# Optimization experiments

Hardware: AMD Instinct MI355X
Metric: run time of the kernel (lower is better)

Reference implementation:

```python
import jax, jax.numpy as jnp
import numpy as np

N = 100000       # nodes
D = 256          # input_dim
H = 256          # hidden = min(2*D, 256)
O = 256          # output_dim
MAXDEG = 16
BN_EPS = 1e-5


def setup_inputs() -> dict:
    key = jax.random.key(0)
    ks = jax.random.split(key, 6)
    x = jax.random.normal(ks[0], (N, D), dtype=jnp.float32)
    padded_neighbors = jax.random.randint(ks[1], (N, MAXDEG), 0, N, dtype=jnp.int32)
    W1 = jax.random.normal(ks[2], (D, H), dtype=jnp.float32) * (1.0 / np.sqrt(D))
    b1 = jnp.zeros((H,), jnp.float32)
    W2 = jax.random.normal(ks[3], (H, O), dtype=jnp.float32) * (1.0 / np.sqrt(H))
    b2 = jnp.zeros((O,), jnp.float32)
    gamma = jnp.ones((O,), jnp.float32)
    beta = jnp.zeros((O,), jnp.float32)
    alpha = jnp.float32(0.1)   # Parameter init in 'mean_max' branch
    eps = jnp.float32(0.0)     # learnable eps, init 0.0
    return {"x": x, "padded_neighbors": padded_neighbors, "W1": W1, "b1": b1,
            "W2": W2, "b2": b2, "gamma": gamma, "beta": beta,
            "alpha": alpha, "eps": eps}


def max_pooling_gin(h, padded_neighbors):
    # dummy row = columnwise min; index -1 maps to the dummy row (torch's h[-1])
    dummy = jnp.min(h, axis=0, keepdims=True)          # (1, D)
    h_with_dummy = jnp.concatenate([h, dummy], axis=0)  # (N+1, D)
    idx = jnp.where(padded_neighbors < 0, h.shape[0], padded_neighbors)
    return jnp.max(h_with_dummy[idx], axis=1)           # (N, D)


def reference(x, padded_neighbors, W1, b1, W2, b2, gamma, beta, alpha, eps):
    # --- aggregation: mean over neighbors (== spmm with binary adj / degree) ---
    mask = padded_neighbors >= 0                         # (N, deg)
    idx = jnp.where(mask, padded_neighbors, 0)
    gathered = x[idx] * mask[..., None].astype(x.dtype)  # (N, deg, D)
    neigh_sum = gathered.sum(axis=1)                     # (N, D)
    degree = mask.sum(axis=1, keepdims=True).astype(x.dtype)
    h = neigh_sum / degree
    # --- '_max' branch: add alpha * gather-max of aggregated features ---
    h = h + alpha * max_pooling_gin(h, padded_neighbors)
    # --- self connection + eps residual ---
    h = h + x + eps * x
    # --- backbone: Linear-ReLU-Linear-ReLU-BatchNorm1d (training-mode stats) ---
    h = jax.nn.relu(h @ W1 + b1)
    h = jax.nn.relu(h @ W2 + b2)
    mean = h.mean(axis=0)
    var = h.var(axis=0)  # biased variance, as torch BN uses for normalization
    out = (h - mean) * jax.lax.rsqrt(var + BN_EPS) * gamma + beta
    return out
```

## Files before the change

### kernel.cpp

```cpp
#include <hip/hip_runtime.h>

typedef __bf16 bf16x8 __attribute__((ext_vector_type(8)));
typedef float  f32x4  __attribute__((ext_vector_type(4)));
typedef _Float16 h2v  __attribute__((ext_vector_type(2)));

__device__ __forceinline__ unsigned short f2bf(float f) {
  unsigned u = __builtin_bit_cast(unsigned, f);
  u += 0x7FFFu + ((u >> 16) & 1u);
  return (unsigned short)(u >> 16);
}
__device__ __forceinline__ float bf2f(unsigned short b) {
  unsigned u = ((unsigned)b) << 16;
  return __builtin_bit_cast(float, u);
}
__device__ __forceinline__ float bflo(unsigned q) {
  return __builtin_bit_cast(float, q << 16);
}
__device__ __forceinline__ float bfhi(unsigned q) {
  return __builtin_bit_cast(float, q & 0xFFFF0000u);
}
__device__ __forceinline__ unsigned pack2bf(float lo, float hi) {
  return (unsigned)f2bf(lo) | ((unsigned)f2bf(hi) << 16);
}

__device__ __forceinline__ float fp8raw(unsigned byte) {
  unsigned b = ((byte & 0x80u) << 24) | ((byte & 0x7Fu) << 20);
  return __builtin_bit_cast(float, b);
}
__device__ __forceinline__ unsigned f2fp8(float v) {
  unsigned b = __builtin_bit_cast(unsigned, v);
  unsigned sg = (b >> 24) & 0x80u;
  float a = __builtin_bit_cast(float, b & 0x7FFFFFFFu) * 0x1p-120f;
  unsigned ab = __builtin_bit_cast(unsigned, a);
  ab += 0x7FFFFu + ((ab >> 20) & 1u);
  return sg | ((ab >> 20) & 0x7Fu);
}
__device__ __forceinline__ h2v pkL(unsigned w) {
  unsigned x = ((w << 8) & 0x80008000u) | ((w << 7) & 0x3F803F80u);
  return __builtin_bit_cast(h2v, x);
}
__device__ __forceinline__ h2v pkH(unsigned w) {
  unsigned x = (w & 0x80008000u) | ((w >> 1) & 0x3F803F80u);
  return __builtin_bit_cast(h2v, x);
}
__device__ __forceinline__ h2v shfl32(h2v a) {
  return __builtin_bit_cast(h2v,
      __shfl_xor(__builtin_bit_cast(unsigned, a), 32));
}

__global__ __launch_bounds__(256) void x2bf_kernel(
    const float* __restrict__ x, unsigned short* __restrict__ xh,
    unsigned char* __restrict__ xq, int total8)
{
  const int i = blockIdx.x * 256 + threadIdx.x;
  if (i >= total8) return;
  const float4* p = (const float4*)x + (long)i * 2;
  float4 a = p[0], b = p[1];
  uint4 o;
  o.x = pack2bf(a.x, a.y); o.y = pack2bf(a.z, a.w);
  o.z = pack2bf(b.x, b.y); o.w = pack2bf(b.z, b.w);
  ((uint4*)xh)[i] = o;
  uint2 q;
  q.x = f2fp8(a.x) | (f2fp8(a.y) << 8) | (f2fp8(a.z) << 16) | (f2fp8(a.w) << 24);
  q.y = f2fp8(b.x) | (f2fp8(b.y) << 8) | (f2fp8(b.z) << 16) | (f2fp8(b.w) << 24);
  ((uint2*)xq)[i] = q;
}

__global__ __launch_bounds__(256) void prep_kernel(
    const float* __restrict__ W1, const float* __restrict__ W2,
    unsigned short* __restrict__ Wt1, unsigned short* __restrict__ Wt2)
{
  const int n = blockIdx.x;
  const int k = threadIdx.x;
  Wt1[n * 256 + k] = f2bf(W1[k * 256 + n]);
  Wt2[n * 256 + k] = f2bf(W2[k * 256 + n]);
}

__global__ __launch_bounds__(256) void aggregate_kernel(
    const unsigned char* __restrict__ xq, const int* __restrict__ nbr,
    unsigned short* __restrict__ h0, unsigned char* __restrict__ h0q, int N)
{
  const int wid  = (blockIdx.x * 256 + threadIdx.x) >> 6;
  const int lane = threadIdx.x & 63;
  if (wid >= N) return;
  const int half = lane >> 5;
  const int l    = lane & 31;
  const int* nb = nbr + (long)wid * 16;
  int4 n0 = ((const int4*)nb)[half * 2];
  int4 n1 = ((const int4*)nb)[half * 2 + 1];
  int v[8] = {n0.x, n0.y, n0.z, n0.w, n1.x, n1.y, n1.z, n1.w};
  int mn = v[0];
#pragma unroll
  for (int t = 1; t < 8; ++t) mn = min(mn, v[t]);

  if (__all(mn >= 0)) {
    uint2 vals[8];
#pragma unroll
    for (int t = 0; t < 8; ++t)
      vals[t] = ((const uint2*)(xq + (long)v[t] * 256))[l];
    h2v s02 = (h2v)0, s13 = (h2v)0, s46 = (h2v)0, s57 = (h2v)0;
#pragma unroll
    for (int t = 0; t < 8; ++t) {
      s02 = s02 + pkL(vals[t].x);
      s13 = s13 + pkH(vals[t].x);
      s46 = s46 + pkL(vals[t].y);
      s57 = s57 + pkH(vals[t].y);
    }
    s02 = s02 + shfl32(s02);
    s13 = s13 + shfl32(s13);
    s46 = s46 + shfl32(s46);
    s57 = s57 + shfl32(s57);
    if (half == 0) {
      float m[8];
      m[0] = (float)s02[0] * 16.f; m[2] = (float)s02[1] * 16.f;
      m[1] = (float)s13[0] * 16.f; m[3] = (float)s13[1] * 16.f;
      m[4] = (float)s46[0] * 16.f; m[6] = (float)s46[1] * 16.f;
      m[5] = (float)s57[0] * 16.f; m[7] = (float)s57[1] * 16.f;
      uint4 o;
      o.x = pack2bf(m[0], m[1]); o.y = pack2bf(m[2], m[3]);
      o.z = pack2bf(m[4], m[5]); o.w = pack2bf(m[6], m[7]);
      ((uint4*)(h0 + (long)wid * 256))[l] = o;
      uint2 q;
      q.x = f2fp8(m[0]) | (f2fp8(m[1]) << 8) | (f2fp8(m[2]) << 16) | (f2fp8(m[3]) << 24);
      q.y = f2fp8(m[4]) | (f2fp8(m[5]) << 8) | (f2fp8(m[6]) << 16) | (f2fp8(m[7]) << 24);
      ((uint2*)(h0q + (long)wid * 256))[l] = q;
    }
    return;
  }
  float wgt[8]; int idx[8];
#pragma unroll
  for (int t = 0; t < 8; ++t) {
    wgt[t] = (v[t] >= 0) ? 1.0f : 0.0f;
    idx[t] = (v[t] >= 0) ? v[t] : 0;
  }
  uint2 vals[8];
#pragma unroll
  for (int t = 0; t < 8; ++t)
    vals[t] = ((const uint2*)(xq + (long)idx[t] * 256))[l];
  float s[8] = {0.f,0.f,0.f,0.f,0.f,0.f,0.f,0.f};
  float cnt = 0.f;
#pragma unroll
  for (int t = 0; t < 8; ++t) {
    const unsigned w0 = vals[t].x, w1 = vals[t].y;
    cnt += wgt[t];
    s[0] = fmaf(wgt[t], fp8raw(w0 & 0xFF), s[0]);
    s[1] = fmaf(wgt[t], fp8raw((w0 >> 8) & 0xFF), s[1]);
    s[2] = fmaf(wgt[t], fp8raw((w0 >> 16) & 0xFF), s[2]);
    s[3] = fmaf(wgt[t], fp8raw(w0 >> 24), s[3]);
    s[4] = fmaf(wgt[t], fp8raw(w1 & 0xFF), s[4]);
    s[5] = fmaf(wgt[t], fp8raw((w1 >> 8) & 0xFF), s[5]);
    s[6] = fmaf(wgt[t], fp8raw((w1 >> 16) & 0xFF), s[6]);
    s[7] = fmaf(wgt[t], fp8raw(w1 >> 24), s[7]);
  }
#pragma unroll
  for (int e = 0; e < 8; ++e) s[e] += __shfl_xor(s[e], 32);
  cnt += __shfl_xor(cnt, 32);
  const float inv = cnt > 0.f ? 0x1p120f / cnt : 0.f;
  if (half == 0) {
    float m[8];
#pragma unroll
    for (int e = 0; e < 8; ++e) m[e] = s[e] * inv;
    uint4 o;
    o.x = pack2bf(m[0], m[1]); o.y = pack2bf(m[2], m[3]);
    o.z = pack2bf(m[4], m[5]); o.w = pack2bf(m[6], m[7]);
    ((uint4*)(h0 + (long)wid * 256))[l] = o;
    uint2 q;
    q.x = f2fp8(m[0]) | (f2fp8(m[1]) << 8) | (f2fp8(m[2]) << 16) | (f2fp8(m[3]) << 24);
    q.y = f2fp8(m[4]) | (f2fp8(m[5]) << 8) | (f2fp8(m[6]) << 16) | (f2fp8(m[7]) << 24);
    ((uint2*)(h0q + (long)wid * 256))[l] = q;
  }
}

__global__ __launch_bounds__(256) void combine_kernel(
    const unsigned short* __restrict__ h0, const unsigned char* __restrict__ h0q,
    const int* __restrict__ nbr, const unsigned short* __restrict__ xh,
    const float* __restrict__ alpha_p, const float* __restrict__ eps_p,
    unsigned short* __restrict__ h1, int N)
{
  const int wid  = (blockIdx.x * 256 + threadIdx.x) >> 6;
  const int lane = threadIdx.x & 63;
  if (wid >= N) return;
  const int half = lane >> 5;
  const int l    = lane & 31;
  const float alpha = *alpha_p;
  const float c     = 1.0f + *eps_p;
  const int* nb = nbr + (long)wid * 16;
  int4 n0 = ((const int4*)nb)[half * 2];
  int4 n1 = ((const int4*)nb)[half * 2 + 1];
  int v[8] = {n0.x, n0.y, n0.z, n0.w, n1.x, n1.y, n1.z, n1.w};
  int mn = v[0];
#pragma unroll
  for (int t = 1; t < 8; ++t) mn = min(mn, v[t]);

  uint4 own = ((const uint4*)(h0 + (long)wid * 256))[l];
  uint4 xv  = ((const uint4*)(xh + (long)wid * 256))[l];

  if (__all(mn >= 0)) {
    uint2 vals[8];
#pragma unroll
    for (int t = 0; t < 8; ++t)
      vals[t] = ((const uint2*)(h0q + (long)v[t] * 256))[l];
    const h2v NEG2 = __builtin_bit_cast(h2v, 0xFC00FC00u);
    h2v m02 = NEG2, m13 = NEG2, m46 = NEG2, m57 = NEG2;
#pragma unroll
    for (int t = 0; t < 8; ++t) {
      m02 = __builtin_elementwise_max(m02, pkL(vals[t].x));
      m13 = __builtin_elementwise_max(m13, pkH(vals[t].x));
      m46 = __builtin_elementwise_max(m46, pkL(vals[t].y));
      m57 = __builtin_elementwise_max(m57, pkH(vals[t].y));
    }
    m02 = __builtin_elementwise_max(m02, shfl32(m02));
    m13 = __builtin_elementwise_max(m13, shfl32(m13));
    m46 = __builtin_elementwise_max(m46, shfl32(m46));
    m57 = __builtin_elementwise_max(m57, shfl32(m57));
    if (half == 0) {
      float mx[8];
      mx[0] = (float)m02[0] * 256.f; mx[2] = (float)m02[1] * 256.f;
      mx[1] = (float)m13[0] * 256.f; mx[3] = (float)m13[1] * 256.f;
      mx[4] = (float)m46[0] * 256.f; mx[6] = (float)m46[1] * 256.f;
      mx[5] = (float)m57[0] * 256.f; mx[7] = (float)m57[1] * 256.f;
      const unsigned* qo = (const unsigned*)&own;
      const unsigned* qx = (const unsigned*)&xv;
      uint4 o;
      unsigned* q = (unsigned*)&o;
#pragma unroll
      for (int w = 0; w < 4; ++w) {
        float rl = bflo(qo[w]) + alpha * mx[2*w]   + c * bflo(qx[w]);
        float rh = bfhi(qo[w]) + alpha * mx[2*w+1] + c * bfhi(qx[w]);
        q[w] = pack2bf(rl, rh);
      }
      ((uint4*)(h1 + (long)wid * 256))[l] = o;
    }
    return;
  }
  float mx[8];
#pragma unroll
  for (int e = 0; e < 8; ++e) mx[e] = -3.402823466e38f;
  {
    float wgt[8]; int idx[8];
#pragma unroll
    for (int t = 0; t < 8; ++t) {
      wgt[t] = (v[t] >= 0) ? 1.0f : 0.0f;
      idx[t] = (v[t] >= 0) ? v[t] : 0;
    }
    uint2 vals[8];
#pragma unroll
    for (int t = 0; t < 8; ++t)
      vals[t] = ((const uint2*)(h0q + (long)idx[t] * 256))[l];
#pragma unroll
    for (int t = 0; t < 8; ++t) {
      const unsigned w0 = vals[t].x, w1 = vals[t].y;
      const bool valid = wgt[t] > 0.f;
      const float NEG = -3.402823466e38f;
      mx[0] = fmaxf(mx[0], valid ? fp8raw(w0 & 0xFF) * 0x1p120f : NEG);
      mx[1] = fmaxf(mx[1], valid ? fp8raw((w0 >> 8) & 0xFF) * 0x1p120f : NEG);
      mx[2] = fmaxf(mx[2], valid ? fp8raw((w0 >> 16) & 0xFF) * 0x1p120f : NEG);
      mx[3] = fmaxf(mx[3], valid ? fp8raw(w0 >> 24) * 0x1p120f : NEG);
      mx[4] = fmaxf(mx[4], valid ? fp8raw(w1 & 0xFF) * 0x1p120f : NEG);
      mx[5] = fmaxf(mx[5], valid ? fp8raw((w1 >> 8) & 0xFF) * 0x1p120f : NEG);
      mx[6] = fmaxf(mx[6], valid ? fp8raw((w1 >> 16) & 0xFF) * 0x1p120f : NEG);
      mx[7] = fmaxf(mx[7], valid ? fp8raw(w1 >> 24) * 0x1p120f : NEG);
    }
  }
#pragma unroll
  for (int e = 0; e < 8; ++e) mx[e] = fmaxf(mx[e], __shfl_xor(mx[e], 32));
  if (half == 0) {
    const unsigned* qo = (const unsigned*)&own;
    const unsigned* qx = (const unsigned*)&xv;
    uint4 o;
    unsigned* q = (unsigned*)&o;
#pragma unroll
    for (int w = 0; w < 4; ++w) {
      float rl = bflo(qo[w]) + alpha * mx[2*w]   + c * bflo(qx[w]);
      float rh = bfhi(qo[w]) + alpha * mx[2*w+1] + c * bfhi(qx[w]);
      q[w] = pack2bf(rl, rh);
    }
    ((uint4*)(h1 + (long)wid * 256))[l] = o;
  }
}

template<int WITH_STATS>
__global__ __launch_bounds__(512, 2) void gemm_w_kernel(
    const unsigned short* __restrict__ A, const unsigned short* __restrict__ Wt,
    const float* __restrict__ bias, unsigned short* __restrict__ Out,
    float* __restrict__ partials, int M, int ntiles)
{
  __shared__ __align__(16) unsigned short lW[256 * 256];
  const int tid  = threadIdx.x;
  const int lane = tid & 63;
  const int wave = tid >> 6;
  const int wrh  = wave >> 2;
  const int wc   = wave & 3;
  const int g = lane >> 4, lr = lane & 15;
  char* lWc = (char*)lW;

  {
    const int row   = tid >> 1;
    const int cbase = (tid & 1) * 256;
    const char* src = (const char*)Wt + row * 512 + cbase;
#pragma unroll
    for (int i = 0; i < 16; ++i) {
      uint4 v = *(const uint4*)(src + i * 16);
      *(uint4*)(lWc + ((row * 512 + cbase + i * 16) ^ ((row & 7) << 4))) = v;
    }
  }
  __syncthreads();

  float bv[4];
#pragma unroll
  for (int nt = 0; nt < 4; ++nt) bv[nt] = bias[wc * 64 + nt * 16 + lr];

  float s[4] = {0.f, 0.f, 0.f, 0.f}, s2[4] = {0.f, 0.f, 0.f, 0.f};
  const char* Ab = (const char*)A;

  for (int tile = blockIdx.x; tile < ntiles; tile += gridDim.x) {
    const long row0 = (long)tile * 128;
    f32x4 acc[4][4] = {};
    const long abase = (row0 + wrh * 64 + lr) * 512 + g * 16;
#pragma unroll
    for (int kk = 0; kk < 8; ++kk) {
      bf16x8 af[4], bq[4];
#pragma unroll
      for (int mt = 0; mt < 4; ++mt)
        af[mt] = *(const bf16x8*)(Ab + abase + mt * (16 * 512) + kk * 64);
#pragma unroll
      for (int nt = 0; nt < 4; ++nt) {
        const int wrow = wc * 64 + nt * 16 + lr;
        bq[nt] = *(const bf16x8*)(lWc +
                   ((wrow * 512 + kk * 64 + g * 16) ^ ((wrow & 7) << 4)));
      }
#pragma unroll
      for (int mt = 0; mt < 4; ++mt)
#pragma unroll
        for (int nt = 0; nt < 4; ++nt)
          acc[mt][nt] = __builtin_amdgcn_mfma_f32_16x16x32_bf16(
              af[mt], bq[nt], acc[mt][nt], 0, 0, 0);
    }
#pragma unroll
    for (int nt = 0; nt < 4; ++nt) {
      const int col = wc * 64 + nt * 16 + lr;
#pragma unroll
      for (int mt = 0; mt < 4; ++mt) {
        f32x4 vv = acc[mt][nt];
        const long rbase = row0 + wrh * 64 + mt * 16 + g * 4;
#pragma unroll
        for (int e = 0; e < 4; ++e) {
          const float val = fmaxf(vv[e] + bv[nt], 0.f);
          Out[(rbase + e) * 256 + col] = f2bf(val);
          if (WITH_STATS) {
            if (rbase + e < M) { s[nt] += val; s2[nt] += val * val; }
          }
        }
      }
    }
  }

  if (WITH_STATS) {
#pragma unroll
    for (int nt = 0; nt < 4; ++nt) {
      s[nt]  += __shfl_xor(s[nt], 16);   s2[nt] += __shfl_xor(s2[nt], 16);
      s[nt]  += __shfl_xor(s[nt], 32);   s2[nt] += __shfl_xor(s2[nt], 32);
    }
    if (g == 0) {
      float* p = partials + (blockIdx.x * 2 + wrh) * 512;
#pragma unroll
      for (int nt = 0; nt < 4; ++nt) {
        const int col = wc * 64 + nt * 16 + lr;
        p[col]       = s[nt];
        p[256 + col] = s2[nt];
      }
    }
  }
}

__global__ __launch_bounds__(256) void bn_finalize_kernel(
    const float* __restrict__ gamma, const float* __restrict__ beta,
    const float* __restrict__ partials, float* __restrict__ stats, int M)
{
  const int n = threadIdx.x;
  float s = 0.f, s2 = 0.f;
  for (int b = 0; b < 512; ++b) {
    s  += partials[b * 512 + n];
    s2 += partials[b * 512 + 256 + n];
  }
  const float invM = 1.0f / (float)M;
  const float mean = s * invM;
  float var = s2 * invM - mean * mean;
  var = fmaxf(var, 0.f);
  const float sc = gamma[n] * rsqrtf(var + 1e-5f);
  stats[512 + n] = sc;
  stats[768 + n] = beta[n] - mean * sc;
}

__global__ __launch_bounds__(256) void bn_norm_kernel(
    const unsigned short* __restrict__ h3, const float* __restrict__ stats,
    float* __restrict__ out, int total8)
{
  const int i = blockIdx.x * 256 + threadIdx.x;
  if (i >= total8) return;
  uint4 v = ((const uint4*)h3)[i];
  const int c = (i * 8) & 255;
  const float4 sc0 = *(const float4*)&stats[512 + c];
  const float4 sc1 = *(const float4*)&stats[516 + c];
  const float4 sh0 = *(const float4*)&stats[768 + c];
  const float4 sh1 = *(const float4*)&stats[772 + c];
  const unsigned short* u = (const unsigned short*)&v;
  float4 o0, o1;
  o0.x = bf2f(u[0]) * sc0.x + sh0.x;
  o0.y = bf2f(u[1]) * sc0.y + sh0.y;
  o0.z = bf2f(u[2]) * sc0.z + sh0.z;
  o0.w = bf2f(u[3]) * sc0.w + sh0.w;
  o1.x = bf2f(u[4]) * sc1.x + sh1.x;
  o1.y = bf2f(u[5]) * sc1.y + sh1.y;
  o1.z = bf2f(u[6]) * sc1.z + sh1.z;
  o1.w = bf2f(u[7]) * sc1.w + sh1.w;
  ((float4*)out)[2 * i]     = o0;
  ((float4*)out)[2 * i + 1] = o1;
}

extern "C" void kernel_launch(void* const* d_in, const int* in_sizes, int n_in,
                              void* d_out, int out_size, void* d_ws, size_t ws_size,
                              hipStream_t stream) {
  const float* x     = (const float*)d_in[0];
  const int*   nbr   = (const int*)d_in[1];
  const float* W1    = (const float*)d_in[2];
  const float* b1    = (const float*)d_in[3];
  const float* W2    = (const float*)d_in[4];
  const float* b2    = (const float*)d_in[5];
  const float* gamma = (const float*)d_in[6];
  const float* beta  = (const float*)d_in[7];
  const float* alpha_p = (const float*)d_in[8];
  const float* eps_p   = (const float*)d_in[9];
  float* out = (float*)d_out;

  const int  N  = in_sizes[0] / 256;
  const long MP = ((long)N + 127) & ~127L;
  const int  ntiles = (int)(MP / 128);

  unsigned short* xh   = (unsigned short*)d_ws;
  unsigned short* bufA = xh + MP * 256;
  unsigned short* bufB = bufA + MP * 256;
  unsigned short* Wt1  = bufB + MP * 256;
  unsigned short* Wt2  = Wt1 + 256 * 256;
  unsigned char*  h0q  = (unsigned char*)(Wt2 + 256 * 256);
  float* partials = (float*)(h0q + MP * 256);
  float* stats    = partials + 512 * 512;
  unsigned char*  xq = (unsigned char*)bufB;

  x2bf_kernel<<<(N * 32 + 255) / 256, 256, 0, stream>>>(x, xh, xq, N * 32);
  prep_kernel<<<256, 256, 0, stream>>>(W1, W2, Wt1, Wt2);
  aggregate_kernel<<<(N + 3) / 4, 256, 0, stream>>>(xq, nbr, bufA, h0q, N);
  combine_kernel<<<(N + 3) / 4, 256, 0, stream>>>(bufA, h0q, nbr, xh,
                                                  alpha_p, eps_p, bufB, N);

  gemm_w_kernel<0><<<256, 512, 0, stream>>>(bufB, Wt1, b1, xh, nullptr, N, ntiles);
  gemm_w_kernel<1><<<256, 512, 0, stream>>>(xh, Wt2, b2, bufA, partials, N, ntiles);

  bn_finalize_kernel<<<1, 256, 0, stream>>>(gamma, beta, partials, stats, N);
  bn_norm_kernel<<<(N * 32 + 255) / 256, 256, 0, stream>>>(bufA, stats, out, N * 32);
}
```

Measured before the change: 319.8 us.

## Drop bf16 aggregate buffer and widen GEMM blocks to 16 waves

The aggregate kernel no longer writes a bf16 copy of the mean-aggregated features. The combine kernel reconstructs its own row from the fp8 buffer, which cuts one write and one read of a full N×256 bf16 tensor. Separately, the GEMM kernels now launch 1024 threads per block (16 waves), each computing a 64×32 output slice instead of 64×64. That halves per-wave accumulator registers and spreads the weight-tile load over more threads. The costs are lower precision in the self term (fp8 instead of bf16) and a launch_bounds of (1024,4) that may constrain registers or occupancy.

```diff
diff --git a/kernel.cpp b/kernel.cpp
--- a/kernel.cpp
+++ b/kernel.cpp
@@ -78,7 +78,7 @@
 
 __global__ __launch_bounds__(256) void aggregate_kernel(
     const unsigned char* __restrict__ xq, const int* __restrict__ nbr,
-    unsigned short* __restrict__ h0, unsigned char* __restrict__ h0q, int N)
+    unsigned char* __restrict__ h0q, int N)
 {
   const int wid  = (blockIdx.x * 256 + threadIdx.x) >> 6;
   const int lane = threadIdx.x & 63;
@@ -116,10 +116,6 @@
       m[1] = (float)s13[0] * 16.f; m[3] = (float)s13[1] * 16.f;
       m[4] = (float)s46[0] * 16.f; m[6] = (float)s46[1] * 16.f;
       m[5] = (float)s57[0] * 16.f; m[7] = (float)s57[1] * 16.f;
-      uint4 o;
-      o.x = pack2bf(m[0], m[1]); o.y = pack2bf(m[2], m[3]);
-      o.z = pack2bf(m[4], m[5]); o.w = pack2bf(m[6], m[7]);
-      ((uint4*)(h0 + (long)wid * 256))[l] = o;
       uint2 q;
       q.x = f2fp8(m[0]) | (f2fp8(m[1]) << 8) | (f2fp8(m[2]) << 16) | (f2fp8(m[3]) << 24);
       q.y = f2fp8(m[4]) | (f2fp8(m[5]) << 8) | (f2fp8(m[6]) << 16) | (f2fp8(m[7]) << 24);
@@ -160,10 +156,6 @@
     float m[8];
 #pragma unroll
     for (int e = 0; e < 8; ++e) m[e] = s[e] * inv;
-    uint4 o;
-    o.x = pack2bf(m[0], m[1]); o.y = pack2bf(m[2], m[3]);
-    o.z = pack2bf(m[4], m[5]); o.w = pack2bf(m[6], m[7]);
-    ((uint4*)(h0 + (long)wid * 256))[l] = o;
     uint2 q;
     q.x = f2fp8(m[0]) | (f2fp8(m[1]) << 8) | (f2fp8(m[2]) << 16) | (f2fp8(m[3]) << 24);
     q.y = f2fp8(m[4]) | (f2fp8(m[5]) << 8) | (f2fp8(m[6]) << 16) | (f2fp8(m[7]) << 24);
@@ -172,10 +164,9 @@
 }
 
 __global__ __launch_bounds__(256) void combine_kernel(
-    const unsigned short* __restrict__ h0, const unsigned char* __restrict__ h0q,
-    const int* __restrict__ nbr, const unsigned short* __restrict__ xh,
-    const float* __restrict__ alpha_p, const float* __restrict__ eps_p,
-    unsigned short* __restrict__ h1, int N)
+    const unsigned char* __restrict__ h0q, const int* __restrict__ nbr,
+    const unsigned short* __restrict__ xh, const float* __restrict__ alpha_p,
+    const float* __restrict__ eps_p, unsigned short* __restrict__ h1, int N)
 {
   const int wid  = (blockIdx.x * 256 + threadIdx.x) >> 6;
   const int lane = threadIdx.x & 63;
@@ -192,8 +183,8 @@
 #pragma unroll
   for (int t = 1; t < 8; ++t) mn = min(mn, v[t]);
 
-  uint4 own = ((const uint4*)(h0 + (long)wid * 256))[l];
-  uint4 xv  = ((const uint4*)(xh + (long)wid * 256))[l];
+  uint2 ownq = ((const uint2*)(h0q + (long)wid * 256))[l];
+  uint4 xv   = ((const uint4*)(xh + (long)wid * 256))[l];
 
   if (__all(mn >= 0)) {
     uint2 vals[8];
@@ -219,14 +210,20 @@
       mx[1] = (float)m13[0] * 256.f; mx[3] = (float)m13[1] * 256.f;
       mx[4] = (float)m46[0] * 256.f; mx[6] = (float)m46[1] * 256.f;
       mx[5] = (float)m57[0] * 256.f; mx[7] = (float)m57[1] * 256.f;
-      const unsigned* qo = (const unsigned*)&own;
+      h2v o02 = pkL(ownq.x), o13 = pkH(ownq.x);
+      h2v o46 = pkL(ownq.y), o57 = pkH(ownq.y);
+      float ov[8];
+      ov[0] = (float)o02[0] * 256.f; ov[2] = (float)o02[1] * 256.f;
+      ov[1] = (float)o13[0] * 256.f; ov[3] = (float)o13[1] * 256.f;
+      ov[4] = (float)o46[0] * 256.f; ov[6] = (float)o46[1] * 256.f;
+      ov[5] = (float)o57[0] * 256.f; ov[7] = (float)o57[1] * 256.f;
       const unsigned* qx = (const unsigned*)&xv;
       uint4 o;
       unsigned* q = (unsigned*)&o;
 #pragma unroll
       for (int w = 0; w < 4; ++w) {
-        float rl = bflo(qo[w]) + alpha * mx[2*w]   + c * bflo(qx[w]);
-        float rh = bfhi(qo[w]) + alpha * mx[2*w+1] + c * bfhi(qx[w]);
+        float rl = ov[2*w]   + alpha * mx[2*w]   + c * bflo(qx[w]);
+        float rh = ov[2*w+1] + alpha * mx[2*w+1] + c * bfhi(qx[w]);
         q[w] = pack2bf(rl, rh);
       }
       ((uint4*)(h1 + (long)wid * 256))[l] = o;
@@ -265,14 +262,22 @@
 #pragma unroll
   for (int e = 0; e < 8; ++e) mx[e] = fmaxf(mx[e], __shfl_xor(mx[e], 32));
   if (half == 0) {
-    const unsigned* qo = (const unsigned*)&own;
+    float ov[8];
+    ov[0] = fp8raw(ownq.x & 0xFF) * 0x1p120f;
+    ov[1] = fp8raw((ownq.x >> 8) & 0xFF) * 0x1p120f;
+    ov[2] = fp8raw((ownq.x >> 16) & 0xFF) * 0x1p120f;
+    ov[3] = fp8raw(ownq.x >> 24) * 0x1p120f;
+    ov[4] = fp8raw(ownq.y & 0xFF) * 0x1p120f;
+    ov[5] = fp8raw((ownq.y >> 8) & 0xFF) * 0x1p120f;
+    ov[6] = fp8raw((ownq.y >> 16) & 0xFF) * 0x1p120f;
+    ov[7] = fp8raw(ownq.y >> 24) * 0x1p120f;
     const unsigned* qx = (const unsigned*)&xv;
     uint4 o;
     unsigned* q = (unsigned*)&o;
 #pragma unroll
     for (int w = 0; w < 4; ++w) {
-      float rl = bflo(qo[w]) + alpha * mx[2*w]   + c * bflo(qx[w]);
-      float rh = bfhi(qo[w]) + alpha * mx[2*w+1] + c * bfhi(qx[w]);
+      float rl = ov[2*w]   + alpha * mx[2*w]   + c * bflo(qx[w]);
+      float rh = ov[2*w+1] + alpha * mx[2*w+1] + c * bfhi(qx[w]);
       q[w] = pack2bf(rl, rh);
     }
     ((uint4*)(h1 + (long)wid * 256))[l] = o;
@@ -280,7 +285,7 @@
 }
 
 template<int WITH_STATS>
-__global__ __launch_bounds__(512, 2) void gemm_w_kernel(
+__global__ __launch_bounds__(1024, 4) void gemm_w_kernel(
     const unsigned short* __restrict__ A, const unsigned short* __restrict__ Wt,
     const float* __restrict__ bias, unsigned short* __restrict__ Out,
     float* __restrict__ partials, int M, int ntiles)
@@ -289,56 +294,56 @@
   const int tid  = threadIdx.x;
   const int lane = tid & 63;
   const int wave = tid >> 6;
-  const int wrh  = wave >> 2;
-  const int wc   = wave & 3;
+  const int wrh  = wave >> 3;
+  const int wc   = wave & 7;
   const int g = lane >> 4, lr = lane & 15;
   char* lWc = (char*)lW;
 
   {
-    const int row   = tid >> 1;
-    const int cbase = (tid & 1) * 256;
+    const int row   = tid >> 2;
+    const int cbase = (tid & 3) * 128;
     const char* src = (const char*)Wt + row * 512 + cbase;
 #pragma unroll
-    for (int i = 0; i < 16; ++i) {
+    for (int i = 0; i < 8; ++i) {
       uint4 v = *(const uint4*)(src + i * 16);
       *(uint4*)(lWc + ((row * 512 + cbase + i * 16) ^ ((row & 7) << 4))) = v;
     }
   }
   __syncthreads();
 
-  float bv[4];
-#pragma unroll
-  for (int nt = 0; nt < 4; ++nt) bv[nt] = bias[wc * 64 + nt * 16 + lr];
-
-  float s[4] = {0.f, 0.f, 0.f, 0.f}, s2[4] = {0.f, 0.f, 0.f, 0.f};
+  float bv[2];
+#pragma unroll
+  for (int nt = 0; nt < 2; ++nt) bv[nt] = bias[wc * 32 + nt * 16 + lr];
+
+  float s[2] = {0.f, 0.f}, s2[2] = {0.f, 0.f};
   const char* Ab = (const char*)A;
 
   for (int tile = blockIdx.x; tile < ntiles; tile += gridDim.x) {
     const long row0 = (long)tile * 128;
-    f32x4 acc[4][4] = {};
+    f32x4 acc[4][2] = {};
     const long abase = (row0 + wrh * 64 + lr) * 512 + g * 16;
 #pragma unroll
     for (int kk = 0; kk < 8; ++kk) {
-      bf16x8 af[4], bq[4];
+      bf16x8 af[4], bq[2];
 #pragma unroll
       for (int mt = 0; mt < 4; ++mt)
         af[mt] = *(const bf16x8*)(Ab + abase + mt * (16 * 512) + kk * 64);
 #pragma unroll
-      for (int nt = 0; nt < 4; ++nt) {
-        const int wrow = wc * 64 + nt * 16 + lr;
+      for (int nt = 0; nt < 2; ++nt) {
+        const int wrow = wc * 32 + nt * 16 + lr;
         bq[nt] = *(const bf16x8*)(lWc +
                    ((wrow * 512 + kk * 64 + g * 16) ^ ((wrow & 7) << 4)));
       }
 #pragma unroll
       for (int mt = 0; mt < 4; ++mt)
 #pragma unroll
-        for (int nt = 0; nt < 4; ++nt)
+        for (int nt = 0; nt < 2; ++nt)
           acc[mt][nt] = __builtin_amdgcn_mfma_f32_16x16x32_bf16(
               af[mt], bq[nt], acc[mt][nt], 0, 0, 0);
     }
 #pragma unroll
-    for (int nt = 0; nt < 4; ++nt) {
-      const int col = wc * 64 + nt * 16 + lr;
+    for (int nt = 0; nt < 2; ++nt) {
+      const int col = wc * 32 + nt * 16 + lr;
 #pragma unroll
       for (int mt = 0; mt < 4; ++mt) {
         f32x4 vv = acc[mt][nt];
@@ -357,15 +362,15 @@
 
   if (WITH_STATS) {
 #pragma unroll
-    for (int nt = 0; nt < 4; ++nt) {
+    for (int nt = 0; nt < 2; ++nt) {
       s[nt]  += __shfl_xor(s[nt], 16);   s2[nt] += __shfl_xor(s2[nt], 16);
       s[nt]  += __shfl_xor(s[nt], 32);   s2[nt] += __shfl_xor(s2[nt], 32);
     }
     if (g == 0) {
       float* p = partials + (blockIdx.x * 2 + wrh) * 512;
 #pragma unroll
-      for (int nt = 0; nt < 4; ++nt) {
-        const int col = wc * 64 + nt * 16 + lr;
+      for (int nt = 0; nt < 2; ++nt) {
+        const int col = wc * 32 + nt * 16 + lr;
         p[col]       = s[nt];
         p[256 + col] = s2[nt];
       }
@@ -449,12 +454,12 @@
 
   x2bf_kernel<<<(N * 32 + 255) / 256, 256, 0, stream>>>(x, xh, xq, N * 32);
   prep_kernel<<<256, 256, 0, stream>>>(W1, W2, Wt1, Wt2);
-  aggregate_kernel<<<(N + 3) / 4, 256, 0, stream>>>(xq, nbr, bufA, h0q, N);
-  combine_kernel<<<(N + 3) / 4, 256, 0, stream>>>(bufA, h0q, nbr, xh,
+  aggregate_kernel<<<(N + 3) / 4, 256, 0, stream>>>(xq, nbr, h0q, N);
+  combine_kernel<<<(N + 3) / 4, 256, 0, stream>>>(h0q, nbr, xh,
                                                   alpha_p, eps_p, bufB, N);
 
-  gemm_w_kernel<0><<<256, 512, 0, stream>>>(bufB, Wt1, b1, xh, nullptr, N, ntiles);
-  gemm_w_kernel<1><<<256, 512, 0, stream>>>(xh, Wt2, b2, bufA, partials, N, ntiles);
+  gemm_w_kernel<0><<<256, 1024, 0, stream>>>(bufB, Wt1, b1, xh, nullptr, N, ntiles);
+  gemm_w_kernel<1><<<256, 1024, 0, stream>>>(xh, Wt2, b2, bufA, partials, N, ntiles);
 
   bn_finalize_kernel<<<1, 256, 0, stream>>>(gamma, beta, partials, stats, N);
   bn_norm_kernel<<<(N * 32 + 255) / 256, 256, 0, stream>>>(bufA, stats, out, N * 32);
```

New measurement: 365.3 us. 1.14x slower.

## Retile GEMMs to 256-row by 128-column tiles with one tile per block

Applied to the files above, without the earlier changes.

Drops the persistent 256-block grid and gives each block one 256-row by half-width (128-column) tile, launching 2*ntiles blocks. Each block now stages only half of W in LDS, so the 128 KB buffer becomes 64 KB and launch bounds rise to allow four blocks per CU. The BN partial-sum layout and the finalize reduction change to match. The aim is better occupancy and load balance across the MI355X CUs. In exchange, each block reloads half of W from global memory, and the A rows are read twice, once per column half, which adds traffic.

```diff
diff --git a/kernel.cpp b/kernel.cpp
--- a/kernel.cpp
+++ b/kernel.cpp
@@ -280,26 +280,28 @@
 }
 
 template<int WITH_STATS>
-__global__ __launch_bounds__(512, 2) void gemm_w_kernel(
+__global__ __launch_bounds__(512, 4) void gemm_w_kernel(
     const unsigned short* __restrict__ A, const unsigned short* __restrict__ Wt,
     const float* __restrict__ bias, unsigned short* __restrict__ Out,
-    float* __restrict__ partials, int M, int ntiles)
-{
-  __shared__ __align__(16) unsigned short lW[256 * 256];
+    float* __restrict__ partials, int M)
+{
+  __shared__ __align__(16) unsigned short lW[128 * 256];
   const int tid  = threadIdx.x;
   const int lane = tid & 63;
   const int wave = tid >> 6;
-  const int wrh  = wave >> 2;
-  const int wc   = wave & 3;
+  const int wm   = wave >> 1;
+  const int wn   = wave & 1;
   const int g = lane >> 4, lr = lane & 15;
+  const int colhalf = blockIdx.x & 1;
+  const long row0   = (long)(blockIdx.x >> 1) * 256;
   char* lWc = (char*)lW;
 
   {
-    const int row   = tid >> 1;
-    const int cbase = (tid & 1) * 256;
-    const char* src = (const char*)Wt + row * 512 + cbase;
-#pragma unroll
-    for (int i = 0; i < 16; ++i) {
+    const int row   = tid >> 2;
+    const int cbase = (tid & 3) * 128;
+    const char* src = (const char*)Wt + (long)(colhalf * 128 + row) * 512 + cbase;
+#pragma unroll
+    for (int i = 0; i < 8; ++i) {
       uint4 v = *(const uint4*)(src + i * 16);
       *(uint4*)(lWc + ((row * 512 + cbase + i * 16) ^ ((row & 7) << 4))) = v;
     }
@@ -308,48 +310,47 @@
 
   float bv[4];
 #pragma unroll
-  for (int nt = 0; nt < 4; ++nt) bv[nt] = bias[wc * 64 + nt * 16 + lr];
+  for (int nt = 0; nt < 4; ++nt)
+    bv[nt] = bias[colhalf * 128 + wn * 64 + nt * 16 + lr];
 
   float s[4] = {0.f, 0.f, 0.f, 0.f}, s2[4] = {0.f, 0.f, 0.f, 0.f};
   const char* Ab = (const char*)A;
 
-  for (int tile = blockIdx.x; tile < ntiles; tile += gridDim.x) {
-    const long row0 = (long)tile * 128;
-    f32x4 acc[4][4] = {};
-    const long abase = (row0 + wrh * 64 + lr) * 512 + g * 16;
-#pragma unroll
-    for (int kk = 0; kk < 8; ++kk) {
-      bf16x8 af[4], bq[4];
-#pragma unroll
-      for (int mt = 0; mt < 4; ++mt)
-        af[mt] = *(const bf16x8*)(Ab + abase + mt * (16 * 512) + kk * 64);
-#pragma unroll
-      for (int nt = 0; nt < 4; ++nt) {
-        const int wrow = wc * 64 + nt * 16 + lr;
-        bq[nt] = *(const bf16x8*)(lWc +
-                   ((wrow * 512 + kk * 64 + g * 16) ^ ((wrow & 7) << 4)));
-      }
-#pragma unroll
-      for (int mt = 0; mt < 4; ++mt)
-#pragma unroll
-        for (int nt = 0; nt < 4; ++nt)
-          acc[mt][nt] = __builtin_amdgcn_mfma_f32_16x16x32_bf16(
-              af[mt], bq[nt], acc[mt][nt], 0, 0, 0);
-    }
+  f32x4 acc[4][4] = {};
+  const long abase = (row0 + wm * 64 + lr) * 512 + g * 16;
+#pragma unroll
+  for (int kk = 0; kk < 8; ++kk) {
+    bf16x8 af[4], bq[4];
+#pragma unroll
+    for (int mt = 0; mt < 4; ++mt)
+      af[mt] = *(const bf16x8*)(Ab + abase + mt * (16 * 512) + kk * 64);
 #pragma unroll
     for (int nt = 0; nt < 4; ++nt) {
-      const int col = wc * 64 + nt * 16 + lr;
-#pragma unroll
-      for (int mt = 0; mt < 4; ++mt) {
-        f32x4 vv = acc[mt][nt];
-        const long rbase = row0 + wrh * 64 + mt * 16 + g * 4;
-#pragma unroll
-        for (int e = 0; e < 4; ++e) {
-          const float val = fmaxf(vv[e] + bv[nt], 0.f);
-          Out[(rbase + e) * 256 + col] = f2bf(val);
-          if (WITH_STATS) {
-            if (rbase + e < M) { s[nt] += val; s2[nt] += val * val; }
-          }
+      const int wrow = wn * 64 + nt * 16 + lr;
+      bq[nt] = *(const bf16x8*)(lWc +
+                 ((wrow * 512 + kk * 64 + g * 16) ^ ((wrow & 7) << 4)));
+    }
+#pragma unroll
+    for (int mt = 0; mt < 4; ++mt)
+#pragma unroll
+      for (int nt = 0; nt < 4; ++nt)
+        acc[mt][nt] = __builtin_amdgcn_mfma_f32_16x16x32_bf16(
+            af[mt], bq[nt], acc[mt][nt], 0, 0, 0);
+  }
+
+#pragma unroll
+  for (int nt = 0; nt < 4; ++nt) {
+    const int col = colhalf * 128 + wn * 64 + nt * 16 + lr;
+#pragma unroll
+    for (int mt = 0; mt < 4; ++mt) {
+      f32x4 vv = acc[mt][nt];
+      const long rbase = row0 + wm * 64 + mt * 16 + g * 4;
+#pragma unroll
+      for (int e = 0; e < 4; ++e) {
+        const float val = fmaxf(vv[e] + bv[nt], 0.f);
+        Out[(rbase + e) * 256 + col] = f2bf(val);
+        if (WITH_STATS) {
+          if (rbase + e < M) { s[nt] += val; s2[nt] += val * val; }
         }
       }
     }
@@ -362,12 +363,12 @@
       s[nt]  += __shfl_xor(s[nt], 32);   s2[nt] += __shfl_xor(s2[nt], 32);
     }
     if (g == 0) {
-      float* p = partials + (blockIdx.x * 2 + wrh) * 512;
+      float* p = partials + ((long)blockIdx.x * 4 + wm) * 256;
 #pragma unroll
       for (int nt = 0; nt < 4; ++nt) {
-        const int col = wc * 64 + nt * 16 + lr;
-        p[col]       = s[nt];
-        p[256 + col] = s2[nt];
+        const int cl = wn * 64 + nt * 16 + lr;
+        p[cl]       = s[nt];
+        p[128 + cl] = s2[nt];
       }
     }
   }
@@ -375,13 +376,21 @@
 
 __global__ __launch_bounds__(256) void bn_finalize_kernel(
     const float* __restrict__ gamma, const float* __restrict__ beta,
-    const float* __restrict__ partials, float* __restrict__ stats, int M)
-{
-  const int n = threadIdx.x;
+    const float* __restrict__ partials, float* __restrict__ stats,
+    int M, int ntiles)
+{
+  const int n  = threadIdx.x;
+  const int ch = n >> 7;
+  const int cl = n & 127;
   float s = 0.f, s2 = 0.f;
-  for (int b = 0; b < 512; ++b) {
-    s  += partials[b * 512 + n];
-    s2 += partials[b * 512 + 256 + n];
+  for (int k = 0; k < ntiles; ++k) {
+    const long bid = (long)(2 * k + ch);
+    const float* p = partials + bid * 4 * 256;
+#pragma unroll
+    for (int wm = 0; wm < 4; ++wm) {
+      s  += p[wm * 256 + cl];
+      s2 += p[wm * 256 + 128 + cl];
+    }
   }
   const float invM = 1.0f / (float)M;
   const float mean = s * invM;
@@ -434,8 +443,8 @@
   float* out = (float*)d_out;
 
   const int  N  = in_sizes[0] / 256;
-  const long MP = ((long)N + 127) & ~127L;
-  const int  ntiles = (int)(MP / 128);
+  const long MP = ((long)N + 255) & ~255L;
+  const int  ntiles = (int)(MP / 256);
 
   unsigned short* xh   = (unsigned short*)d_ws;
   unsigned short* bufA = xh + MP * 256;
@@ -444,7 +453,7 @@
   unsigned short* Wt2  = Wt1 + 256 * 256;
   unsigned char*  h0q  = (unsigned char*)(Wt2 + 256 * 256);
   float* partials = (float*)(h0q + MP * 256);
-  float* stats    = partials + 512 * 512;
+  float* stats    = partials + (long)2 * ntiles * 4 * 256;
   unsigned char*  xq = (unsigned char*)bufB;
 
   x2bf_kernel<<<(N * 32 + 255) / 256, 256, 0, stream>>>(x, xh, xq, N * 32);
@@ -453,9 +462,9 @@
   combine_kernel<<<(N + 3) / 4, 256, 0, stream>>>(bufA, h0q, nbr, xh,
                                                   alpha_p, eps_p, bufB, N);
 
-  gemm_w_kernel<0><<<256, 512, 0, stream>>>(bufB, Wt1, b1, xh, nullptr, N, ntiles);
-  gemm_w_kernel<1><<<256, 512, 0, stream>>>(xh, Wt2, b2, bufA, partials, N, ntiles);
-
-  bn_finalize_kernel<<<1, 256, 0, stream>>>(gamma, beta, partials, stats, N);
+  gemm_w_kernel<0><<<2 * ntiles, 512, 0, stream>>>(bufB, Wt1, b1, xh, nullptr, N);
+  gemm_w_kernel<1><<<2 * ntiles, 512, 0, stream>>>(xh, Wt2, b2, bufA, partials, N);
+
+  bn_finalize_kernel<<<1, 256, 0, stream>>>(gamma, beta, partials, stats, N, ntiles);
   bn_norm_kernel<<<(N * 32 + 255) / 256, 256, 0, stream>>>(bufA, stats, out, N * 32);
 }
```

New measurement: 422.2 us. 32.0% more time.
